# Performance work log

Measured on AMD Instinct MI355X. Metric: run time of the kernel, lower is better.

The kernel has to match this reference:

```python
import jax, jax.numpy as jnp
import numpy as np

N_NODES = 5000
N_EDGES = 80000
IN_DIM = 128
HID_DIM = 128
OUT_DIM = 64
NUM_HEADS = 1
BATCH = 8
NEG_SLOPE = 0.2  # DGL GATConv default leaky_relu negative_slope


def setup_inputs() -> dict:
    key = jax.random.key(0)
    ks = jax.random.split(key, 12)
    x = jax.random.normal(ks[0], (BATCH, N_NODES, IN_DIM), dtype=jnp.float32)
    src = jax.random.randint(ks[1], (N_EDGES,), 0, N_NODES)
    dst = jax.random.randint(ks[2], (N_EDGES,), 0, N_NODES)
    # layer1 params (fc has no bias in DGL GATConv; output bias present by default)
    s1 = 1.0 / np.sqrt(IN_DIM)
    W1 = jax.random.normal(ks[3], (IN_DIM, NUM_HEADS * HID_DIM), dtype=jnp.float32) * s1
    al1 = jax.random.normal(ks[4], (NUM_HEADS, HID_DIM), dtype=jnp.float32) * 0.1
    ar1 = jax.random.normal(ks[5], (NUM_HEADS, HID_DIM), dtype=jnp.float32) * 0.1
    b1 = jnp.zeros((NUM_HEADS * HID_DIM,), dtype=jnp.float32)
    # layer2 params
    s2 = 1.0 / np.sqrt(NUM_HEADS * HID_DIM)
    W2 = jax.random.normal(ks[6], (NUM_HEADS * HID_DIM, NUM_HEADS * OUT_DIM), dtype=jnp.float32) * s2
    al2 = jax.random.normal(ks[7], (NUM_HEADS, OUT_DIM), dtype=jnp.float32) * 0.1
    ar2 = jax.random.normal(ks[8], (NUM_HEADS, OUT_DIM), dtype=jnp.float32) * 0.1
    b2 = jnp.zeros((NUM_HEADS * OUT_DIM,), dtype=jnp.float32)
    return {"x": x, "W1": W1, "al1": al1, "ar1": ar1, "b1": b1,
            "W2": W2, "al2": al2, "ar2": ar2, "b2": b2,
            "src": src, "dst": dst}


def gat_layer(x, W, al, ar, b, src, dst, n_nodes):
    """DGL GATConv. x:[B,N,Din] W:[Din,H*F] al/ar:[H,F] b:[H*F] -> [B,N,H,F]."""
    B = x.shape[0]
    H, F = al.shape
    z = (x @ W).reshape(B, n_nodes, H, F)                 # [B,N,H,F]
    el = jnp.einsum('bnhf,hf->bnh', z, al)                # src-side attn term
    er = jnp.einsum('bnhf,hf->bnh', z, ar)                # dst-side attn term
    e = jax.nn.leaky_relu(el[:, src] + er[:, dst], NEG_SLOPE)  # [B,E,H]
    e = jnp.moveaxis(e, 1, 0)                             # [E,B,H]  edge-major for segment ops
    emax = jax.ops.segment_max(e, dst, num_segments=n_nodes)   # [N,B,H]
    ex = jnp.exp(e - emax[dst])
    denom = jax.ops.segment_sum(ex, dst, num_segments=n_nodes)  # [N,B,H]
    alpha = ex / denom[dst]                               # edge softmax over incoming edges
    zs = jnp.moveaxis(z[:, src], 1, 0)                    # [E,B,H,F] gathered source feats
    out = jax.ops.segment_sum(alpha[..., None] * zs, dst, num_segments=n_nodes)  # [N,B,H,F]
    return jnp.moveaxis(out, 0, 1) + b.reshape(1, 1, H, F)


def reference(x, W1, al1, ar1, b1, W2, al2, ar2, b2, src, dst):
    n_nodes = x.shape[1]
    h = gat_layer(x, W1, al1, ar1, b1, src, dst, n_nodes)  # [B,N,H,hid]
    B, N, H, Fh = h.shape
    h = h.reshape(B, N, H * Fh)                            # concat heads (H=1)
    o = gat_layer(h, W2, al2, ar2, b2, src, dst, n_nodes)  # [B,N,H,out]
    o = o.reshape(B * N, -1)                               # squeeze: [B*N, out]
    return jax.nn.softmax(o, axis=-1)
```

## Files before the change

### kernel.cpp

```cpp
#include <hip/hip_runtime.h>
#include <hip/hip_bf16.h>

#define N_NODES 5000
#define N_EDGES 80000
#define HID_DIM 128
#define OUT_DIM 64
#define BATCH 8
#define M_ROWS 40000
#define NEG_SLOPE 0.2f
#define BUCKET 96


typedef unsigned short ushort_t;
typedef unsigned int uint_t;
typedef __attribute__((ext_vector_type(8))) short short8;
typedef __attribute__((ext_vector_type(4))) float f32x4;

__device__ __forceinline__ float bf16_to_f32(ushort_t u) {
  return __uint_as_float(((uint_t)u) << 16);
}
__device__ __forceinline__ ushort_t f32_to_bf16(float f) {
  uint_t u = __float_as_uint(f);
  return (ushort_t)((u + 0x7FFF + ((u >> 16) & 1)) >> 16);
}

struct __attribute__((aligned(8))) us4 { ushort_t x, y, z, w; };

#define OFF_BP1   0u
#define OFF_BP2   32768u
#define OFF_CMETA 49152u
#define OFF_CB    49184u
#define OFF_Y     65536u
#define OFF_EY    5185536u
#define OFF_W     5505536u
#define OFF_EL1   10625536u
#define OFF_ER1   10785536u
#define OFF_EL2   10945536u
#define OFF_ER2   11105536u
#define OFF_CNT   11265536u
#define OFF_SRCS  11285536u

__global__ __launch_bounds__(256) void zero_pack_kernel(const float* __restrict__ W1,
                                                        const float* __restrict__ W2,
                                                        const float* __restrict__ b1,
                                                        const float* __restrict__ b2,
                                                        const float* __restrict__ al2,
                                                        const float* __restrict__ ar2,
                                                        int* __restrict__ cnt,
                                                        ushort_t* __restrict__ Bp1,
                                                        ushort_t* __restrict__ Bp2,
                                                        float* __restrict__ cmeta,
                                                        float* __restrict__ cb) {
  int bid = blockIdx.x;
  if (bid < 20) {
    int i = bid * 256 + threadIdx.x;
    if (i < N_NODES) cnt[i] = 0;
    return;
  }
  if (bid == 32) {
    int f = threadIdx.x;
    if (f < 64) {
      float c = 0.f;
#pragma unroll 8
      for (int k = 0; k < 128; k++) c += b1[k] * W2[(size_t)k * 64 + f];
      cb[f] = c + b2[f];
      float cl = c * al2[f], cr = c * ar2[f];
#pragma unroll
      for (int o = 32; o; o >>= 1) {
        cl += __shfl_xor(cl, o, 64);
        cr += __shfl_xor(cr, o, 64);
      }
      if (f == 0) { cmeta[0] = cl; cmeta[1] = cr; }
    }
    return;
  }
  int gid = (bid - 20) * 256 + threadIdx.x;
  if (gid >= 3072) return;
  const float* W; ushort_t* Bp; int NC, idx;
  if (gid < 2048) { W = W1; Bp = Bp1; NC = 128; idx = gid; }
  else            { W = W2; Bp = Bp2; NC = 64;  idx = gid - 2048; }
  int l = idx & 63, tt = idx >> 6;
  int T = NC / 16;
  int kc = tt / T, t = tt % T;
  int col = t * 16 + (l & 15);
  int krow = kc * 32 + (l >> 4) * 8;
  short8 vv;
#pragma unroll
  for (int j = 0; j < 8; j++) vv[j] = (short)f32_to_bf16(W[(size_t)(krow + j) * NC + col]);
  *(short8*)(Bp + (size_t)idx * 8) = vv;
}

__global__ __launch_bounds__(256) void gemm_fused(const float* __restrict__ A,
                                                  const ushort_t* __restrict__ Bp1,
                                                  const ushort_t* __restrict__ Bp2,
                                                  const float* __restrict__ al1,
                                                  const float* __restrict__ ar1,
                                                  const float* __restrict__ al2,
                                                  const float* __restrict__ ar2,
                                                  float* __restrict__ el1,
                                                  float* __restrict__ er1,
                                                  ushort_t* __restrict__ y,
                                                  float2* __restrict__ ey,
                                                  const int* __restrict__ e_src,
                                                  const int* __restrict__ e_dst,
                                                  int* __restrict__ cnt,
                                                  int* __restrict__ srcs) {
  {
    int tid = threadIdx.x;
    if (tid < 128) {
      int i = blockIdx.x * 128 + tid;
      int d = e_dst[i];
      int pos = atomicAdd(&cnt[d], 1);
      if (pos < BUCKET) srcs[d * BUCKET + pos] = e_src[i];
    }
  }
  __shared__ ushort_t lds[64 * 128];
  int wave = threadIdx.x >> 6, lane = threadIdx.x & 63;
  int q = lane >> 4, m = lane & 15;
  int r0 = blockIdx.x * 64 + wave * 16;

  f32x4 acc[8];
#pragma unroll
  for (int t = 0; t < 8; t++)
#pragma unroll
    for (int i = 0; i < 4; i++) acc[t][i] = 0.f;
  const short8* B1 = (const short8*)Bp1;
  size_t arow = (size_t)(r0 + m) * 128;
#pragma unroll
  for (int kc = 0; kc < 4; kc++) {
    const float* Ap = A + arow + kc * 32 + q * 8;
    float4 v0 = *(const float4*)Ap;
    float4 v1 = *(const float4*)(Ap + 4);
    short8 af;
    af[0] = (short)f32_to_bf16(v0.x); af[1] = (short)f32_to_bf16(v0.y);
    af[2] = (short)f32_to_bf16(v0.z); af[3] = (short)f32_to_bf16(v0.w);
    af[4] = (short)f32_to_bf16(v1.x); af[5] = (short)f32_to_bf16(v1.y);
    af[6] = (short)f32_to_bf16(v1.z); af[7] = (short)f32_to_bf16(v1.w);
#pragma unroll
    for (int t = 0; t < 8; t++)
      acc[t] = __builtin_amdgcn_mfma_f32_16x16x32_bf16(af, B1[(kc * 8 + t) * 64 + lane], acc[t], 0, 0, 0);
  }
  {
    float sl[4] = {0.f, 0.f, 0.f, 0.f}, sr[4] = {0.f, 0.f, 0.f, 0.f};
#pragma unroll
    for (int t = 0; t < 8; t++) {
      float alv = al1[t * 16 + m], arv = ar1[t * 16 + m];
#pragma unroll
      for (int i = 0; i < 4; i++) { sl[i] += acc[t][i] * alv; sr[i] += acc[t][i] * arv; }
    }
#pragma unroll
    for (int o = 1; o < 16; o <<= 1)
#pragma unroll
      for (int i = 0; i < 4; i++) {
        sl[i] += __shfl_xor(sl[i], o, 64);
        sr[i] += __shfl_xor(sr[i], o, 64);
      }
    if (m == 0)
#pragma unroll
      for (int i = 0; i < 4; i++) {
        el1[r0 + q * 4 + i] = sl[i];
        er1[r0 + q * 4 + i] = sr[i];
      }
  }
#pragma unroll
  for (int t = 0; t < 8; t++)
#pragma unroll
    for (int i = 0; i < 4; i++) {
      int row = q * 4 + i + wave * 16;
      int byte = row * 256 + (t * 16 + m) * 2;
      lds[(byte ^ ((row & 7) << 4)) >> 1] = f32_to_bf16(acc[t][i]);
    }
  __syncthreads();

  f32x4 acc2[4];
#pragma unroll
  for (int t = 0; t < 4; t++)
#pragma unroll
    for (int i = 0; i < 4; i++) acc2[t][i] = 0.f;
  const short8* B2 = (const short8*)Bp2;
  int row2 = wave * 16 + m;
#pragma unroll
  for (int kc = 0; kc < 4; kc++) {
    int byte = row2 * 256 + kc * 64 + q * 16;
    short8 af2 = *(const short8*)((const char*)lds + (byte ^ ((row2 & 7) << 4)));
#pragma unroll
    for (int t = 0; t < 4; t++)
      acc2[t] = __builtin_amdgcn_mfma_f32_16x16x32_bf16(af2, B2[(kc * 4 + t) * 64 + lane], acc2[t], 0, 0, 0);
  }
  {
    float sl[4] = {0.f, 0.f, 0.f, 0.f}, sr[4] = {0.f, 0.f, 0.f, 0.f};
#pragma unroll
    for (int t = 0; t < 4; t++) {
      float alv = al2[t * 16 + m], arv = ar2[t * 16 + m];
#pragma unroll
      for (int i = 0; i < 4; i++) { sl[i] += acc2[t][i] * alv; sr[i] += acc2[t][i] * arv; }
    }
#pragma unroll
    for (int o = 1; o < 16; o <<= 1)
#pragma unroll
      for (int i = 0; i < 4; i++) {
        sl[i] += __shfl_xor(sl[i], o, 64);
        sr[i] += __shfl_xor(sr[i], o, 64);
      }
    if (m == 0)
#pragma unroll
      for (int i = 0; i < 4; i++) ey[r0 + q * 4 + i] = make_float2(sl[i], sr[i]);
  }
#pragma unroll
  for (int t = 0; t < 4; t++)
#pragma unroll
    for (int i = 0; i < 4; i++)
      y[(size_t)(r0 + q * 4 + i) * 64 + t * 16 + m] = f32_to_bf16(acc2[t][i]);
}

__global__ __launch_bounds__(256) void agg_mid(const ushort_t* __restrict__ y,
                                               const float2* __restrict__ ey,
                                               const float* __restrict__ el,
                                               const float* __restrict__ er,
                                               const int* __restrict__ cnt,
                                               const int* __restrict__ srcs,
                                               const float* __restrict__ cmeta,
                                               ushort_t* __restrict__ w,
                                               float* __restrict__ el2,
                                               float* __restrict__ er2) {
  int id = (threadIdx.x >> 6) * gridDim.x + blockIdx.x;
  int lane = threadIdx.x & 63;
  int g = lane >> 4, l16 = lane & 15;
  int b = id & 7, n = id >> 3;
  int deg = cnt[n]; if (deg > BUCKET) deg = BUCKET;
  int off0 = n * BUCKET;
  int rbase = b * N_NODES;
  float er_n = er[rbase + n];

  float acc[4] = {0.f, 0.f, 0.f, 0.f};
  float lsum = 0.f, sl2 = 0.f, sr2 = 0.f;

  for (int c = 0; c < deg; c += 64) {
    int j = c + lane;
    int s_my = 0;
    float w_my = 0.f;
    if (j < deg) {
      s_my = srcs[off0 + j];
      float e = el[rbase + s_my] + er_n;
      e = e > 0.f ? e : NEG_SLOPE * e;
      w_my = __expf(e);
      lsum += w_my;
      float2 ev = ey[rbase + s_my];
      sl2 += w_my * ev.x;
      sr2 += w_my * ev.y;
    }
    int cl = deg - c; if (cl > 64) cl = 64;
    for (int k0 = 0; k0 < cl; k0 += 16) {
      float wk[4]; int sk[4];
#pragma unroll
      for (int u = 0; u < 4; u++) {
        int e_idx = k0 + u * 4 + g;
        wk[u] = __shfl(w_my, e_idx, 64);
        sk[u] = __shfl(s_my, e_idx, 64);
      }
      uint2 zw[4];
#pragma unroll
      for (int u = 0; u < 4; u++)
        zw[u] = *(const uint2*)(y + (size_t)(rbase + sk[u]) * 64 + l16 * 4);
#pragma unroll
      for (int u = 0; u < 4; u++) {
        acc[0] += wk[u] * bf16_to_f32((ushort_t)(zw[u].x & 0xFFFF));
        acc[1] += wk[u] * bf16_to_f32((ushort_t)(zw[u].x >> 16));
        acc[2] += wk[u] * bf16_to_f32((ushort_t)(zw[u].y & 0xFFFF));
        acc[3] += wk[u] * bf16_to_f32((ushort_t)(zw[u].y >> 16));
      }
    }
  }
#pragma unroll
  for (int j = 0; j < 4; j++) {
    acc[j] += __shfl_xor(acc[j], 16, 64);
    acc[j] += __shfl_xor(acc[j], 32, 64);
  }
  float sum = lsum;
#pragma unroll
  for (int o = 32; o; o >>= 1) {
    sum += __shfl_xor(sum, o, 64);
    sl2 += __shfl_xor(sl2, o, 64);
    sr2 += __shfl_xor(sr2, o, 64);
  }
  float inv = (deg > 0) ? 1.f / sum : 0.f;

  if (g == 0) {
    uint_t pk0 = (uint_t)f32_to_bf16(acc[0] * inv) | ((uint_t)f32_to_bf16(acc[1] * inv) << 16);
    uint_t pk1 = (uint_t)f32_to_bf16(acc[2] * inv) | ((uint_t)f32_to_bf16(acc[3] * inv) << 16);
    *(uint2*)(w + (size_t)(rbase + n) * 64 + l16 * 4) = make_uint2(pk0, pk1);
  }
  if (lane == 0) {
    el2[rbase + n] = sl2 * inv + cmeta[0];
    er2[rbase + n] = sr2 * inv + cmeta[1];
  }
}

__global__ __launch_bounds__(256) void agg_fin(const ushort_t* __restrict__ w,
                                               const float* __restrict__ el,
                                               const float* __restrict__ er,
                                               const float* __restrict__ cb,
                                               const int* __restrict__ cnt,
                                               const int* __restrict__ srcs,
                                               float* __restrict__ outp) {
  int id = (threadIdx.x >> 6) * gridDim.x + blockIdx.x;
  int lane = threadIdx.x & 63;
  int g = lane >> 4, l16 = lane & 15;
  int b = id & 7, n = id >> 3;
  int deg = cnt[n]; if (deg > BUCKET) deg = BUCKET;
  int off0 = n * BUCKET;
  int rbase = b * N_NODES;
  float er_n = er[rbase + n];

  float acc[4] = {0.f, 0.f, 0.f, 0.f};
  float lsum = 0.f;

  for (int c = 0; c < deg; c += 64) {
    int j = c + lane;
    int s_my = 0;
    float w_my = 0.f;
    if (j < deg) {
      s_my = srcs[off0 + j];
      float e = el[rbase + s_my] + er_n;
      e = e > 0.f ? e : NEG_SLOPE * e;
      w_my = __expf(e);
      lsum += w_my;
    }
    int cl = deg - c; if (cl > 64) cl = 64;
    for (int k0 = 0; k0 < cl; k0 += 16) {
      float wk[4]; int sk[4];
#pragma unroll
      for (int u = 0; u < 4; u++) {
        int e_idx = k0 + u * 4 + g;
        wk[u] = __shfl(w_my, e_idx, 64);
        sk[u] = __shfl(s_my, e_idx, 64);
      }
      uint2 zw[4];
#pragma unroll
      for (int u = 0; u < 4; u++)
        zw[u] = *(const uint2*)(w + (size_t)(rbase + sk[u]) * 64 + l16 * 4);
#pragma unroll
      for (int u = 0; u < 4; u++) {
        acc[0] += wk[u] * bf16_to_f32((ushort_t)(zw[u].x & 0xFFFF));
        acc[1] += wk[u] * bf16_to_f32((ushort_t)(zw[u].x >> 16));
        acc[2] += wk[u] * bf16_to_f32((ushort_t)(zw[u].y & 0xFFFF));
        acc[3] += wk[u] * bf16_to_f32((ushort_t)(zw[u].y >> 16));
      }
    }
  }
#pragma unroll
  for (int j = 0; j < 4; j++) {
    acc[j] += __shfl_xor(acc[j], 16, 64);
    acc[j] += __shfl_xor(acc[j], 32, 64);
  }
  float sum = lsum;
#pragma unroll
  for (int o = 32; o; o >>= 1) sum += __shfl_xor(sum, o, 64);
  float inv = (deg > 0) ? 1.f / sum : 0.f;

  float o[4];
#pragma unroll
  for (int j = 0; j < 4; j++) o[j] = acc[j] * inv + cb[l16 * 4 + j];
  float mm = fmaxf(fmaxf(o[0], o[1]), fmaxf(o[2], o[3]));
#pragma unroll
  for (int d = 1; d < 16; d <<= 1) mm = fmaxf(mm, __shfl_xor(mm, d, 64));
  float p0 = __expf(o[0] - mm), p1 = __expf(o[1] - mm);
  float p2 = __expf(o[2] - mm), p3 = __expf(o[3] - mm);
  float ss = p0 + p1 + p2 + p3;
#pragma unroll
  for (int d = 1; d < 16; d <<= 1) ss += __shfl_xor(ss, d, 64);
  if (g == 0) {
    float issv = 1.f / ss;
    *(float4*)(outp + (size_t)(rbase + n) * 64 + l16 * 4) =
        make_float4(p0 * issv, p1 * issv, p2 * issv, p3 * issv);
  }
}

extern "C" void kernel_launch(void* const* d_in, const int* in_sizes, int n_in,
                              void* d_out, int out_size, void* d_ws, size_t ws_size,
                              hipStream_t stream) {
  const float* x   = (const float*)d_in[0];
  const float* W1  = (const float*)d_in[1];
  const float* al1 = (const float*)d_in[2];
  const float* ar1 = (const float*)d_in[3];
  const float* b1  = (const float*)d_in[4];
  const float* W2  = (const float*)d_in[5];
  const float* al2 = (const float*)d_in[6];
  const float* ar2 = (const float*)d_in[7];
  const float* b2  = (const float*)d_in[8];
  const int* src = (const int*)d_in[9];
  const int* dst = (const int*)d_in[10];

  char* base = (char*)d_ws;
  ushort_t* Bp1  = (ushort_t*)(base + OFF_BP1);
  ushort_t* Bp2  = (ushort_t*)(base + OFF_BP2);
  float*    cmeta= (float*)(base + OFF_CMETA);
  float*    cb   = (float*)(base + OFF_CB);
  ushort_t* y    = (ushort_t*)(base + OFF_Y);
  float2*   ey   = (float2*)(base + OFF_EY);
  ushort_t* w    = (ushort_t*)(base + OFF_W);
  float* el1 = (float*)(base + OFF_EL1);
  float* er1 = (float*)(base + OFF_ER1);
  float* el2 = (float*)(base + OFF_EL2);
  float* er2 = (float*)(base + OFF_ER2);
  int* cnt  = (int*)(base + OFF_CNT);
  int* srcs = (int*)(base + OFF_SRCS);

  zero_pack_kernel<<<33, 256, 0, stream>>>(W1, W2, b1, b2, al2, ar2, cnt, Bp1, Bp2, cmeta, cb);

  gemm_fused<<<M_ROWS / 64, 256, 0, stream>>>(x, Bp1, Bp2, al1, ar1, al2, ar2,
                                              el1, er1, y, ey, src, dst, cnt, srcs);

  agg_mid<<<M_ROWS / 4, 256, 0, stream>>>(y, ey, el1, er1, cnt, srcs, cmeta, w, el2, er2);

  agg_fin<<<M_ROWS / 4, 256, 0, stream>>>(w, el2, er2, cb, cnt, srcs, (float*)d_out);
}
```

Measured before the change: 143.3 us.

## Fold weight packing into GEMM kernel via LDS and replace zero kernel with memset

```diff
diff --git a/kernel.cpp b/kernel.cpp
--- a/kernel.cpp
+++ b/kernel.cpp
@@ -24,10 +24,6 @@
   return (ushort_t)((u + 0x7FFF + ((u >> 16) & 1)) >> 16);
 }
 
-struct __attribute__((aligned(8))) us4 { ushort_t x, y, z, w; };
-
-#define OFF_BP1   0u
-#define OFF_BP2   32768u
 #define OFF_CMETA 49152u
 #define OFF_CB    49184u
 #define OFF_Y     65536u
@@ -40,59 +36,11 @@
 #define OFF_CNT   11265536u
 #define OFF_SRCS  11285536u
 
-__global__ __launch_bounds__(256) void zero_pack_kernel(const float* __restrict__ W1,
-                                                        const float* __restrict__ W2,
-                                                        const float* __restrict__ b1,
-                                                        const float* __restrict__ b2,
-                                                        const float* __restrict__ al2,
-                                                        const float* __restrict__ ar2,
-                                                        int* __restrict__ cnt,
-                                                        ushort_t* __restrict__ Bp1,
-                                                        ushort_t* __restrict__ Bp2,
-                                                        float* __restrict__ cmeta,
-                                                        float* __restrict__ cb) {
-  int bid = blockIdx.x;
-  if (bid < 20) {
-    int i = bid * 256 + threadIdx.x;
-    if (i < N_NODES) cnt[i] = 0;
-    return;
-  }
-  if (bid == 32) {
-    int f = threadIdx.x;
-    if (f < 64) {
-      float c = 0.f;
-#pragma unroll 8
-      for (int k = 0; k < 128; k++) c += b1[k] * W2[(size_t)k * 64 + f];
-      cb[f] = c + b2[f];
-      float cl = c * al2[f], cr = c * ar2[f];
-#pragma unroll
-      for (int o = 32; o; o >>= 1) {
-        cl += __shfl_xor(cl, o, 64);
-        cr += __shfl_xor(cr, o, 64);
-      }
-      if (f == 0) { cmeta[0] = cl; cmeta[1] = cr; }
-    }
-    return;
-  }
-  int gid = (bid - 20) * 256 + threadIdx.x;
-  if (gid >= 3072) return;
-  const float* W; ushort_t* Bp; int NC, idx;
-  if (gid < 2048) { W = W1; Bp = Bp1; NC = 128; idx = gid; }
-  else            { W = W2; Bp = Bp2; NC = 64;  idx = gid - 2048; }
-  int l = idx & 63, tt = idx >> 6;
-  int T = NC / 16;
-  int kc = tt / T, t = tt % T;
-  int col = t * 16 + (l & 15);
-  int krow = kc * 32 + (l >> 4) * 8;
-  short8 vv;
-#pragma unroll
-  for (int j = 0; j < 8; j++) vv[j] = (short)f32_to_bf16(W[(size_t)(krow + j) * NC + col]);
-  *(short8*)(Bp + (size_t)idx * 8) = vv;
-}
-
 __global__ __launch_bounds__(256) void gemm_fused(const float* __restrict__ A,
-                                                  const ushort_t* __restrict__ Bp1,
-                                                  const ushort_t* __restrict__ Bp2,
+                                                  const float* __restrict__ W1,
+                                                  const float* __restrict__ W2,
+                                                  const float* __restrict__ b1,
+                                                  const float* __restrict__ b2,
                                                   const float* __restrict__ al1,
                                                   const float* __restrict__ ar1,
                                                   const float* __restrict__ al2,
@@ -104,27 +52,61 @@
                                                   const int* __restrict__ e_src,
                                                   const int* __restrict__ e_dst,
                                                   int* __restrict__ cnt,
-                                                  int* __restrict__ srcs) {
-  {
-    int tid = threadIdx.x;
-    if (tid < 128) {
-      int i = blockIdx.x * 128 + tid;
-      int d = e_dst[i];
-      int pos = atomicAdd(&cnt[d], 1);
-      if (pos < BUCKET) srcs[d * BUCKET + pos] = e_src[i];
-    }
-  }
+                                                  int* __restrict__ srcs,
+                                                  float* __restrict__ cmeta,
+                                                  float* __restrict__ cb) {
+  __shared__ ushort_t ldsB1[2048 * 8];
+  __shared__ ushort_t ldsB2[1024 * 8];
   __shared__ ushort_t lds[64 * 128];
   int wave = threadIdx.x >> 6, lane = threadIdx.x & 63;
   int q = lane >> 4, m = lane & 15;
   int r0 = blockIdx.x * 64 + wave * 16;
 
+  if (threadIdx.x < 128) {
+    int i = blockIdx.x * 128 + threadIdx.x;
+    int d = e_dst[i];
+    int pos = atomicAdd(&cnt[d], 1);
+    if (pos < BUCKET) srcs[d * BUCKET + pos] = e_src[i];
+  }
+
+  for (int it = 0; it < 12; it++) {
+    int gid = it * 256 + threadIdx.x;
+    const float* W; ushort_t* Bp; int NC, idx;
+    if (gid < 2048) { W = W1; Bp = ldsB1; NC = 128; idx = gid; }
+    else            { W = W2; Bp = ldsB2; NC = 64;  idx = gid - 2048; }
+    int l = idx & 63, tt = idx >> 6;
+    int T = NC / 16;
+    int kc = tt / T, t = tt % T;
+    int col = t * 16 + (l & 15);
+    int krow = kc * 32 + (l >> 4) * 8;
+    short8 vv;
+#pragma unroll
+    for (int j = 0; j < 8; j++) vv[j] = (short)f32_to_bf16(W[(size_t)(krow + j) * NC + col]);
+    *(short8*)(Bp + (size_t)idx * 8) = vv;
+  }
+
+  if (blockIdx.x == 0 && threadIdx.x < 64) {
+    int f = threadIdx.x;
+    float c = 0.f;
+#pragma unroll 8
+    for (int k = 0; k < 128; k++) c += b1[k] * W2[(size_t)k * 64 + f];
+    cb[f] = c + b2[f];
+    float cl = c * al2[f], cr = c * ar2[f];
+#pragma unroll
+    for (int o = 32; o; o >>= 1) {
+      cl += __shfl_xor(cl, o, 64);
+      cr += __shfl_xor(cr, o, 64);
+    }
+    if (f == 0) { cmeta[0] = cl; cmeta[1] = cr; }
+  }
+  __syncthreads();
+
   f32x4 acc[8];
 #pragma unroll
   for (int t = 0; t < 8; t++)
 #pragma unroll
     for (int i = 0; i < 4; i++) acc[t][i] = 0.f;
-  const short8* B1 = (const short8*)Bp1;
+  const short8* B1 = (const short8*)ldsB1;
   size_t arow = (size_t)(r0 + m) * 128;
 #pragma unroll
   for (int kc = 0; kc < 4; kc++) {
@@ -177,7 +159,7 @@
   for (int t = 0; t < 4; t++)
 #pragma unroll
     for (int i = 0; i < 4; i++) acc2[t][i] = 0.f;
-  const short8* B2 = (const short8*)Bp2;
+  const short8* B2 = (const short8*)ldsB2;
   int row2 = wave * 16 + m;
 #pragma unroll
   for (int kc = 0; kc < 4; kc++) {
@@ -392,8 +374,6 @@
   const int* dst = (const int*)d_in[10];
 
   char* base = (char*)d_ws;
-  ushort_t* Bp1  = (ushort_t*)(base + OFF_BP1);
-  ushort_t* Bp2  = (ushort_t*)(base + OFF_BP2);
   float*    cmeta= (float*)(base + OFF_CMETA);
   float*    cb   = (float*)(base + OFF_CB);
   ushort_t* y    = (ushort_t*)(base + OFF_Y);
@@ -406,10 +386,11 @@
   int* cnt  = (int*)(base + OFF_CNT);
   int* srcs = (int*)(base + OFF_SRCS);
 
-  zero_pack_kernel<<<33, 256, 0, stream>>>(W1, W2, b1, b2, al2, ar2, cnt, Bp1, Bp2, cmeta, cb);
-
-  gemm_fused<<<M_ROWS / 64, 256, 0, stream>>>(x, Bp1, Bp2, al1, ar1, al2, ar2,
-                                              el1, er1, y, ey, src, dst, cnt, srcs);
+  hipMemsetAsync(cnt, 0, N_NODES * sizeof(int), stream);
+
+  gemm_fused<<<M_ROWS / 64, 256, 0, stream>>>(x, W1, W2, b1, b2, al1, ar1, al2, ar2,
+                                              el1, er1, y, ey, src, dst, cnt, srcs,
+                                              cmeta, cb);
 
   agg_mid<<<M_ROWS / 4, 256, 0, stream>>>(y, ey, el1, er1, cnt, srcs, cmeta, w, el2, er2);
 
```

Result: slower. 146.8 us (+2.4%).
